# Kernel tuning notes

Hardware: AMD Instinct MI355X
Metric: run time of the kernel (lower is better)

## Reference

```python
import jax, jax.numpy as jnp
import numpy as np

# dims (Nemotron-H 8B class mamba mixer)
HID = 4096      # hidden_size
NH = 128        # mamba_num_heads
HD = 64         # mamba_head_dim
DIN = NH * HD   # intermediate_size = 8192
G = 8           # n_groups
N = 128         # ssm_state_size
K = 4           # conv_kernel
CS = 256        # chunk_size
EPS = 1e-5
GROUP_SIZE = DIN // G
CONV_DIM = DIN + 2 * G * N           # 10240
PROJ = DIN + CONV_DIM + NH           # 18560 = gate | xBC | dt


def segment_sum(x):
    """x: [..., k] -> [..., k, k]; out[i,j] = sum_{m=j+1..i} x[m], -inf above diag."""
    k = x.shape[-1]
    xe = jnp.broadcast_to(x[..., None], x.shape + (k,))
    xe = jnp.where(jnp.tril(jnp.ones((k, k), bool), -1), xe, 0.0)
    s = jnp.cumsum(xe, axis=-2)
    return jnp.where(jnp.tril(jnp.ones((k, k), bool), 0), s, -jnp.inf)


def setup_inputs() -> dict:
    key = jax.random.key(0)
    ks = jax.random.split(key, 9)
    std = 0.02
    return {
        "hidden_states": jax.random.normal(ks[0], (2, 2048, HID), jnp.float32),
        "in_proj_w": jax.random.normal(ks[1], (PROJ, HID), jnp.float32) * std,
        "conv_w": jax.random.normal(ks[2], (CONV_DIM, 1, K), jnp.float32) * 0.1,
        "conv_b": jax.random.normal(ks[3], (CONV_DIM,), jnp.float32) * 0.01,
        "dt_bias": jax.random.uniform(ks[4], (NH,), jnp.float32, -4.0, -2.0),
        "A_log": jnp.log(jax.random.uniform(ks[5], (NH,), jnp.float32, 1.0, 16.0)),
        "D": jnp.ones((NH,), jnp.float32),
        "norm_w": jnp.ones((DIN,), jnp.float32),
        "out_proj_w": jax.random.normal(ks[8], (HID, DIN), jnp.float32) * std,
    }


def reference(hidden_states, in_proj_w, conv_w, conv_b, dt_bias, A_log, D, norm_w, out_proj_w):
    b, l, _ = hidden_states.shape
    zxbcdt = hidden_states @ in_proj_w.T                       # [b,l,PROJ]
    gate = zxbcdt[..., :DIN]
    xBC = zxbcdt[..., DIN:DIN + CONV_DIM]
    dt = zxbcdt[..., DIN + CONV_DIM:]                          # [b,l,NH]

    # causal depthwise conv1d + silu
    conv = jax.lax.conv_general_dilated(
        jnp.transpose(xBC, (0, 2, 1)), conv_w, (1,), [(K - 1, 0)],
        feature_group_count=CONV_DIM, dimension_numbers=("NCH", "OIH", "NCH"))
    xBC = jax.nn.silu(jnp.transpose(conv + conv_b[None, :, None], (0, 2, 1)))

    x = xBC[..., :DIN].reshape(b, l, NH, HD)
    B = xBC[..., DIN:DIN + G * N].reshape(b, l, G, N)
    C = xBC[..., DIN + G * N:].reshape(b, l, G, N)
    B = jnp.repeat(B, NH // G, axis=2)                         # [b,l,NH,N]
    C = jnp.repeat(C, NH // G, axis=2)

    A = -jnp.exp(A_log)                                        # [NH]
    dt = jax.nn.softplus(dt + dt_bias)                         # [b,l,NH]; limit (0,inf) is a no-op

    pad = (CS - l % CS) % CS
    def padl(t):
        return jnp.pad(t, [(0, 0), (0, pad)] + [(0, 0)] * (t.ndim - 2))

    D_res = D[None, None, :, None] * padl(x)                   # [b,L,NH,HD]
    xs = x * dt[..., None]
    Adt = A[None, None, :] * dt                                # [b,l,NH]

    nc = (l + pad) // CS
    def chunk(t):
        return padl(t).reshape((b, nc, CS) + t.shape[2:])
    xs, B, C = chunk(xs), chunk(B), chunk(C)                   # [b,c,k,h,*]
    Ac = jnp.transpose(chunk(Adt), (0, 3, 1, 2))               # [b,h,c,k]
    A_cumsum = jnp.cumsum(Ac, axis=-1)

    # 1. intra-chunk (diagonal blocks)
    L = jnp.exp(segment_sum(Ac))                               # [b,h,c,k,k]
    Gm = jnp.einsum("bcihn,bcjhn->bhcij", C, B)
    Y_diag = jnp.einsum("bhcij,bcjhd->bcihd", Gm * L, xs)

    # 2. chunk states
    decay_states = jnp.exp(A_cumsum[..., -1:] - A_cumsum)      # [b,h,c,k]
    states = jnp.einsum("bckhn,bhck,bckhd->bchdn", B, decay_states, xs)

    # 3. inter-chunk recurrence
    A_tail = jnp.pad(A_cumsum[..., -1], ((0, 0), (0, 0), (1, 0)))
    decay_chunk = jnp.exp(segment_sum(A_tail))                 # [b,h,c+1,c+1]
    states = jnp.concatenate([jnp.zeros_like(states[:, :1]), states], axis=1)
    new_states = jnp.einsum("bhzc,bchdn->bzhdn", decay_chunk, states)
    states = new_states[:, :-1]                                # [b,c,h,d,n]

    # 4. state -> output
    state_decay = jnp.exp(A_cumsum)                            # [b,h,c,k]
    Y_off = jnp.einsum("bckhn,bchdn,bhck->bckhd", C, states, state_decay)

    y = (Y_diag + Y_off).reshape(b, l + pad, NH, HD) + D_res
    y = y[:, :l].reshape(b, l, DIN)

    # gated grouped RMSNorm
    y = y * jax.nn.silu(gate)
    yg = y.reshape(b, l, G, GROUP_SIZE)
    var = jnp.mean(yg * yg, axis=-1, keepdims=True)
    y = (yg * jax.lax.rsqrt(var + EPS)).reshape(b, l, DIN) * norm_w
    return y @ out_proj_w.T
```

## Files before the change

kernel.cpp:

```cpp
#include <hip/hip_runtime.h>
#include <hip/hip_bf16.h>
#include <math.h>

#define HID 4096
#define NH 128
#define HD 64
#define DIN 8192
#define G 8
#define NSTATE 128
#define CS 256
#define GROUP_SIZE 1024
#define CONV_DIM 10240
#define ZXW 18432
#define BATCH 2
#define SEQ 2048
#define NT (BATCH*SEQ)
#define NC 8
#define DTSK 16

typedef __attribute__((ext_vector_type(8))) short bf16x8;
typedef __attribute__((ext_vector_type(4))) float f32x4;
typedef __attribute__((ext_vector_type(8))) unsigned short u16x8;
typedef __attribute__((ext_vector_type(4))) unsigned short u16x4;

__device__ __forceinline__ float sigmoidf_(float x){ return 1.f/(1.f+expf(-x)); }
__device__ __forceinline__ float siluf_(float x){ return x*sigmoidf_(x); }
__device__ __forceinline__ float softplusf_(float x){ return (x>20.f)? x : log1pf(expf(x)); }
__device__ __forceinline__ float b2f(unsigned short u){ union{unsigned int i; float f;} x; x.i = ((unsigned int)u)<<16; return x.f; }
__device__ __forceinline__ unsigned short f2b(float f){ __hip_bfloat16 h = __float2bfloat16(f); return *(unsigned short*)&h; }

__device__ __forceinline__ void gload_lds16(const void* g, void* l) {
  __builtin_amdgcn_global_load_lds((const __attribute__((address_space(1))) unsigned int*)g,
                                   (__attribute__((address_space(3))) unsigned int*)l, 16, 0, 0);
}
__device__ __forceinline__ bf16x8 ld8bf(const __hip_bfloat16* p){ return *(const bf16x8*)p; }

__device__ __forceinline__ void cast8(const float* in, __hip_bfloat16* out) {
  const float4* p = (const float4*)in;
  float4 a = p[0], b = p[1];
  union { __hip_bfloat16 h[8]; int4 v; } o;
  o.h[0]=__float2bfloat16(a.x); o.h[1]=__float2bfloat16(a.y);
  o.h[2]=__float2bfloat16(a.z); o.h[3]=__float2bfloat16(a.w);
  o.h[4]=__float2bfloat16(b.x); o.h[5]=__float2bfloat16(b.y);
  o.h[6]=__float2bfloat16(b.z); o.h[7]=__float2bfloat16(b.w);
  *(int4*)out = o.v;
}

__global__ __launch_bounds__(256)
void cast2_kernel(const float* __restrict__ w_in, __hip_bfloat16* __restrict__ w_in_bf,
                  const float* __restrict__ w_out, __hip_bfloat16* __restrict__ w_out_bf) {
  const size_t n1 = (size_t)ZXW*HID/8;
  const size_t n2 = (size_t)HID*DIN/8;
  const size_t ntot = n1 + n2;
  size_t i = (size_t)blockIdx.x * 256 + threadIdx.x;
  size_t stride = (size_t)gridDim.x * 256;
  for (; i < ntot; i += stride) {
    if (i < n1)  cast8(w_in + i*8,      w_in_bf + i*8);
    else         cast8(w_out+ (i-n1)*8, w_out_bf+ (i-n1)*8);
  }
}

template<bool OUT_BF16>
__global__ __launch_bounds__(512)
void gemm_bf16_256(const __hip_bfloat16* __restrict__ A, const __hip_bfloat16* __restrict__ B,
                   void* __restrict__ Cout, int M, int N, int K) {
  const int nMt = M >> 8, nNt = N >> 8;
  const int nwg = nMt * nNt;
  const int cpx = nwg >> 3;
  const int lin = blockIdx.x;
  const int swz = (lin & 7) * cpx + (lin >> 3);
  const int mt = swz % nMt, ntile = swz / nMt;
  const int rowBase = mt << 8;
  const int colBase = ntile << 8;

  __shared__ short As[4][8192];
  __shared__ short Bs[4][8192];

  const int tid = threadIdx.x;
  const int lane = tid & 63, wid = tid >> 6;
  const int wr = wid >> 2, wc = wid & 3;
  const int l15 = lane & 15, l4 = lane >> 4;

  const int r0 = tid >> 2,        c0 = (tid & 3) ^ ((r0 >> 1) & 3);
  const int r1 = (512+tid) >> 2,  c1 = ((512+tid) & 3) ^ ((r1 >> 1) & 3);
  const __hip_bfloat16* gA0 = A + (size_t)(rowBase + r0)*K + c0*8;
  const __hip_bfloat16* gA1 = A + (size_t)(rowBase + r1)*K + c1*8;
  const __hip_bfloat16* gB0 = B + (size_t)(colBase + r0)*K + c0*8;
  const __hip_bfloat16* gB1 = B + (size_t)(colBase + r1)*K + c1*8;
  const int ld0 = wid*512, ld1 = 4096 + wid*512;

#define STAGE_A(q, kt) do { \
    gload_lds16(gA0 + (size_t)(kt)*32, (void*)&As[q][ld0]); \
    gload_lds16(gA1 + (size_t)(kt)*32, (void*)&As[q][ld1]); \
  } while(0)
#define STAGE_B(q, kt) do { \
    gload_lds16(gB0 + (size_t)(kt)*32, (void*)&Bs[q][ld0]); \
    gload_lds16(gB1 + (size_t)(kt)*32, (void*)&Bs[q][ld1]); \
  } while(0)

  int aoff[8], boff[4];
  #pragma unroll
  for (int m=0;m<8;++m){ int r = wr*128 + m*16 + l15; aoff[m] = r*32 + ((l4 ^ ((r>>1)&3))*8); }
  #pragma unroll
  for (int n=0;n<4;++n){ int r = wc*64  + n*16 + l15; boff[n] = r*32 + ((l4 ^ ((r>>1)&3))*8); }

  f32x4 acc[8][4] = {};
  const int NKT = K >> 5;

  STAGE_A(0,0); STAGE_B(0,0);
  STAGE_A(1,1); STAGE_B(1,1);
  STAGE_A(2,2); STAGE_B(2,2);
  asm volatile("s_waitcnt vmcnt(8)" ::: "memory");
  __builtin_amdgcn_s_barrier();

  for (int t = 0; t < NKT; ++t) {
    const short* ab = &As[t&3][0];
    const short* bb = &Bs[t&3][0];
    const int q3 = (t+3)&3;
    bf16x8 a[4], b[4], a2[4];
    #pragma unroll
    for (int m=0;m<4;++m) a[m] = *(const bf16x8*)&ab[aoff[m]];
    #pragma unroll
    for (int n=0;n<4;++n) b[n] = *(const bf16x8*)&bb[boff[n]];
    if (t + 3 < NKT) STAGE_A(q3, t+3);
    __builtin_amdgcn_s_barrier();
    asm volatile("s_waitcnt lgkmcnt(0)" ::: "memory");
    __builtin_amdgcn_sched_barrier(0);
    __builtin_amdgcn_s_setprio(1);
    #pragma unroll
    for (int m=0;m<4;++m)
      #pragma unroll
      for (int n=0;n<4;++n)
        acc[m][n] = __builtin_amdgcn_mfma_f32_16x16x32_bf16(a[m], b[n], acc[m][n], 0, 0, 0);
    __builtin_amdgcn_s_setprio(0);
    __builtin_amdgcn_s_barrier();
    #pragma unroll
    for (int m=0;m<4;++m) a2[m] = *(const bf16x8*)&ab[aoff[m+4]];
    if (t + 3 < NKT) STAGE_B(q3, t+3);
    const int rem = NKT - 1 - t;
    if (rem >= 3)      asm volatile("s_waitcnt vmcnt(8)" ::: "memory");
    else if (rem == 2) asm volatile("s_waitcnt vmcnt(4)" ::: "memory");
    else if (rem == 1) asm volatile("s_waitcnt vmcnt(0)" ::: "memory");
    __builtin_amdgcn_s_barrier();
    asm volatile("s_waitcnt lgkmcnt(0)" ::: "memory");
    __builtin_amdgcn_sched_barrier(0);
    __builtin_amdgcn_s_setprio(1);
    #pragma unroll
    for (int m=0;m<4;++m)
      #pragma unroll
      for (int n=0;n<4;++n)
        acc[m+4][n] = __builtin_amdgcn_mfma_f32_16x16x32_bf16(a2[m], b[n], acc[m+4][n], 0, 0, 0);
    __builtin_amdgcn_s_setprio(0);
    __builtin_amdgcn_s_barrier();
  }
#undef STAGE_A
#undef STAGE_B

  #pragma unroll
  for (int m=0;m<8;++m) {
    int row0 = rowBase + wr*128 + m*16 + l4*4;
    #pragma unroll
    for (int n=0;n<4;++n) {
      int col = colBase + wc*64 + n*16 + l15;
      #pragma unroll
      for (int j=0;j<4;++j) {
        if (OUT_BF16)
          ((__hip_bfloat16*)Cout)[(size_t)(row0+j)*N + col] = __float2bfloat16(acc[m][n][j]);
        else
          ((float*)Cout)[(size_t)(row0+j)*N + col] = acc[m][n][j];
      }
    }
  }
}

__global__ __launch_bounds__(256)
void dt_gemm_splitk(const float* __restrict__ A, const float* __restrict__ B,
                    float* __restrict__ partial, __hip_bfloat16* __restrict__ hs_bf) {
  __shared__ float As[16][132];
  __shared__ float Bs[16][132];
  const int tid = threadIdx.x;
  const int tx = tid & 15, ty = tid >> 4;
  const int rowBase = blockIdx.y * 128;
  const int k0 = blockIdx.x * (HID/DTSK);
  float acc[8][8] = {};
  for (int kt = k0; kt < k0 + HID/DTSK; kt += 16) {
    for (int e = tid; e < 128*16; e += 256) {
      int r = e >> 4, c = e & 15;
      float av = A[(size_t)(rowBase + r) * HID + kt + c];
      As[c][r] = av;
      hs_bf[(size_t)(rowBase + r) * HID + kt + c] = __float2bfloat16(av);
      Bs[c][r] = B[(size_t)r * HID + kt + c];
    }
    __syncthreads();
    #pragma unroll
    for (int kk = 0; kk < 16; ++kk) {
      float a[8], bv[8];
      #pragma unroll
      for (int i = 0; i < 8; ++i) a[i] = As[kk][ty*8+i];
      #pragma unroll
      for (int j = 0; j < 8; ++j) bv[j] = Bs[kk][tx*8+j];
      #pragma unroll
      for (int i = 0; i < 8; ++i)
        #pragma unroll
        for (int j = 0; j < 8; ++j)
          acc[i][j] += a[i]*bv[j];
    }
    __syncthreads();
  }
  float* outp = partial + (size_t)blockIdx.x * NT * NH;
  for (int i = 0; i < 8; ++i) {
    size_t ro = (size_t)(rowBase + ty*8 + i) * NH + tx*8;
    #pragma unroll
    for (int j = 0; j < 8; ++j) outp[ro + j] = acc[i][j];
  }
}

__global__ __launch_bounds__(256)
void dt_scan_kernel(const float* __restrict__ partial, const float* __restrict__ dt_bias,
                    const float* __restrict__ A_log, float* __restrict__ dt_sp,
                    float* __restrict__ Acs) {
  int bid = blockIdx.x;
  int c = bid % NC;
  int h = (bid / NC) % NH;
  int b = bid / (NC*NH);
  int k = threadIdx.x;
  int t = b*SEQ + c*CS + k;
  float raw = dt_bias[h];
  #pragma unroll
  for (int sk = 0; sk < DTSK; ++sk) raw += partial[(size_t)sk*NT*NH + (size_t)t*NH + h];
  float dtv = softplusf_(raw);
  dt_sp[(size_t)t*NH + h] = dtv;
  float adt = -expf(A_log[h]) * dtv;
  __shared__ float s[CS];
  s[k] = adt;
  __syncthreads();
  for (int off = 1; off < CS; off <<= 1) {
    float v = (k >= off) ? s[k-off] : 0.f;
    __syncthreads();
    s[k] += v;
    __syncthreads();
  }
  Acs[((size_t)(b*NH + h)*NC + c)*CS + k] = s[k];
}

__global__ __launch_bounds__(256)
void conv_fused_kernel(const __hip_bfloat16* __restrict__ zx, const float* __restrict__ w,
                       const float* __restrict__ bias,
                       const float* __restrict__ dt_sp, const float* __restrict__ Acs,
                       __hip_bfloat16* __restrict__ xsT, __hip_bfloat16* __restrict__ xwT,
                       __hip_bfloat16* __restrict__ Bbf, __hip_bfloat16* __restrict__ Cbf,
                       __hip_bfloat16* __restrict__ BT) {
  const int tt = blockIdx.x;
  const int ct = blockIdx.y;
  const int t0 = tt*64;
  const int ch0 = ct*64;
  const int tid = threadIdx.x;
  __shared__ unsigned short T[64][72];
  __shared__ float dts[64], ews[64];

  const bool isX = (ch0 < DIN);
  const bool isB = (ch0 >= DIN) && (ch0 < DIN + G*NSTATE);

  if (isX && tid < 64) {
    int h = ch0 >> 6;
    int t = t0 + tid;
    dts[tid] = dt_sp[(size_t)t*NH + h];
    int b = t0 >> 11, cc = (t0 >> 8) & 7, k0 = t0 & 255;
    const float* acs = Acs + ((size_t)(b*NH+h)*NC + cc)*CS;
    ews[tid] = __expf(acs[CS-1] - acs[k0 + tid]);
  }

  const int l0 = t0 & (SEQ-1);
  #pragma unroll
  for (int it = 0; it < 2; ++it) {
    int r = tid >> 2;
    int c8 = (tid & 3) + it*4;
    int cb = ch0 + c8*8;
    float acc[8];
    *(float4*)&acc[0] = *(const float4*)&bias[cb];
    *(float4*)&acc[4] = *(const float4*)&bias[cb+4];
    float4 wv[8];
    #pragma unroll
    for (int q=0;q<8;++q) wv[q] = *(const float4*)&w[(cb+q)*4];
    #pragma unroll
    for (int k=0;k<4;++k) {
      if (l0 + r - 3 + k >= 0) {
        u16x8 v = *(const u16x8*)&zx[(size_t)(t0+r-3+k)*ZXW + DIN + cb];
        #pragma unroll
        for (int q=0;q<8;++q) acc[q] += b2f(v[q]) * ((const float*)&wv[q])[k];
      }
    }
    u16x8 o;
    #pragma unroll
    for (int q=0;q<8;++q) o[q] = f2b(siluf_(acc[q]));
    if (isX || isB) {
      #pragma unroll
      for (int q=0;q<8;++q) T[c8*8+q][r] = o[q];
    }
    if (!isX) {
      if (isB) *(u16x8*)&Bbf[(size_t)(t0+r)*(G*NSTATE) + (cb - DIN)] = o;
      else     *(u16x8*)&Cbf[(size_t)(t0+r)*(G*NSTATE) + (cb - DIN - G*NSTATE)] = o;
    }
  }
  if (!isX && !isB) return;
  __syncthreads();
  #pragma unroll
  for (int it = 0; it < 2; ++it) {
    int ch = tid >> 2;
    int tc = (tid & 3) + it*4;
    u16x8 v = *(const u16x8*)&T[ch][tc*8];
    if (isX) {
      u16x8 a, wv2;
      #pragma unroll
      for (int q=0;q<8;++q) {
        float f = b2f(v[q]);
        float fs = f * dts[tc*8+q];
        a[q]   = f2b(fs);
        wv2[q] = f2b(fs * ews[tc*8+q]);
      }
      *(u16x8*)&xsT[(size_t)(ch0+ch)*NT + t0 + tc*8] = a;
      *(u16x8*)&xwT[(size_t)(ch0+ch)*NT + t0 + tc*8] = wv2;
    } else {
      *(u16x8*)&BT[(size_t)(ch0 - DIN + ch)*NT + t0 + tc*8] = v;
    }
  }
}

__global__ __launch_bounds__(256)
void chunk_states_fused(const __hip_bfloat16* __restrict__ xwT, const __hip_bfloat16* __restrict__ BT,
                        const float* __restrict__ Acs, __hip_bfloat16* __restrict__ states_bf) {
  int h = blockIdx.x, b = blockIdx.y;
  int g = h >> 4;
  int tid = threadIdx.x, lane = tid & 63, w = tid >> 6;
  int l15 = lane & 15, l4 = lane >> 4;
  int n0 = w*32;
  f32x4 S[4][2] = {};
  for (int c = 0; c < NC; ++c) {
    int tbase = b*SEQ + c*CS;
    const __hip_bfloat16* xp = xwT + (size_t)(h*64 + l15)*NT + tbase + l4*8;
    const __hip_bfloat16* bp = BT + (size_t)(g*128 + n0 + l15)*NT + tbase + l4*8;
    f32x4 acc[4][2] = {};
    for (int kc = 0; kc < 8; ++kc) {
      bf16x8 xf[4], bf2[2];
      #pragma unroll
      for (int tm=0;tm<4;++tm) xf[tm] = ld8bf(xp + (size_t)(tm*16)*NT + kc*32);
      #pragma unroll
      for (int tn=0;tn<2;++tn) bf2[tn] = ld8bf(bp + (size_t)(tn*16)*NT + kc*32);
      #pragma unroll
      for (int tm=0;tm<4;++tm)
        #pragma unroll
        for (int tn=0;tn<2;++tn)
          acc[tm][tn] = __builtin_amdgcn_mfma_f32_16x16x32_bf16(xf[tm], bf2[tn], acc[tm][tn], 0, 0, 0);
    }
    __hip_bfloat16* out = states_bf + ((size_t)(b*NC + c)*NH + h)*(HD*NSTATE);
    float decay = expf(Acs[((size_t)(b*NH+h)*NC + c)*CS + CS-1]);
    #pragma unroll
    for (int tm=0;tm<4;++tm)
      #pragma unroll
      for (int tn=0;tn<2;++tn)
        #pragma unroll
        for (int q=0;q<4;++q) {
          out[(size_t)(tm*16 + l4*4 + q)*NSTATE + n0 + tn*16 + l15] = __float2bfloat16(S[tm][tn][q]);
          S[tm][tn][q] = S[tm][tn][q]*decay + acc[tm][tn][q];
        }
  }
}

__global__ __launch_bounds__(256)
void y_mfma_kernel(const __hip_bfloat16* __restrict__ zx,
                   const __hip_bfloat16* __restrict__ Cn,
                   const __hip_bfloat16* __restrict__ Bn,
                   const __hip_bfloat16* __restrict__ xsT,
                   const __hip_bfloat16* __restrict__ Sbf,
                   const float* __restrict__ dt_sp,
                   const float* __restrict__ Acs,
                   const float* __restrict__ Dp,
                   __hip_bfloat16* __restrict__ ybf) {
  int h = blockIdx.x;
  int bc = blockIdx.y;
  int c = bc & 7, b = bc >> 3;
  int g = h >> 4;
  int tbase = b*SEQ + c*CS;
  int tid = threadIdx.x, lane = tid & 63, w = tid >> 6;
  int l15 = lane & 15, l4 = lane >> 4;
  int i0 = w*64;
  __shared__ float acs_s[CS];
  __shared__ unsigned short P[4][64][72];
  acs_s[tid] = Acs[((size_t)(b*NH+h)*NC + c)*CS + tid];
  __syncthreads();

  float acs_i[4], rd[4];
  float Dh = Dp[h];
  #pragma unroll
  for (int ti=0;ti<4;++ti) {
    int ig = i0 + ti*16 + l15;
    acs_i[ti] = acs_s[ig];
    rd[ti] = Dh / dt_sp[(size_t)(tbase+ig)*NH + h];
  }
  const __hip_bfloat16* Cbase = Cn + (size_t)tbase*1024 + g*128;
  const __hip_bfloat16* Bbase = Bn + (size_t)tbase*1024 + g*128;
  const __hip_bfloat16* xbase = xsT + (size_t)(h*64 + l15)*NT + tbase;

  bf16x8 cfr[4][4];
  #pragma unroll
  for (int kc = 0; kc < 4; ++kc)
    #pragma unroll
    for (int ti=0;ti<4;++ti)
      cfr[kc][ti] = ld8bf(Cbase + (size_t)(i0 + ti*16 + l15)*1024 + kc*32 + l4*8);

  f32x4 accY[4][4] = {};
  for (int jb = 0; jb <= w; ++jb) {
    int j0 = jb*64;
    f32x4 sacc[4][4] = {};
    for (int kc = 0; kc < 4; ++kc) {
      bf16x8 bfr[4];
      #pragma unroll
      for (int tj=0;tj<4;++tj) bfr[tj] = ld8bf(Bbase + (size_t)(j0 + tj*16 + l15)*1024 + kc*32 + l4*8);
      #pragma unroll
      for (int tj=0;tj<4;++tj)
        #pragma unroll
        for (int ti=0;ti<4;++ti)
          sacc[tj][ti] = __builtin_amdgcn_mfma_f32_16x16x32_bf16(bfr[tj], cfr[kc][ti], sacc[tj][ti], 0, 0, 0);
    }
    if (jb < w) {
      #pragma unroll
      for (int tj=0;tj<4;++tj)
        #pragma unroll
        for (int ti=0;ti<4;++ti) {
          float ai = acs_i[ti];
          u16x4 pk;
          #pragma unroll
          for (int q=0;q<4;++q) {
            int jg = j0 + tj*16 + l4*4 + q;
            pk[q] = f2b(sacc[tj][ti][q] * __expf(ai - acs_s[jg]));
          }
          *(u16x4*)&P[w][ti*16 + l15][tj*16 + l4*4] = pk;
        }
    } else {
      #pragma unroll
      for (int tj=0;tj<4;++tj)
        #pragma unroll
        for (int ti=0;ti<4;++ti) {
          int ig = i0 + ti*16 + l15;
          float ai = acs_i[ti];
          u16x4 pk;
          #pragma unroll
          for (int q=0;q<4;++q) {
            int jg = j0 + tj*16 + l4*4 + q;
            float v = (jg <= ig) ? sacc[tj][ti][q] * __expf(ai - acs_s[jg]) : 0.f;
            if (jg == ig) v += rd[ti];
            pk[q] = f2b(v);
          }
          *(u16x4*)&P[w][ti*16 + l15][tj*16 + l4*4] = pk;
        }
    }
    #pragma unroll
    for (int kc2 = 0; kc2 < 2; ++kc2) {
      bf16x8 xf[4], pf[4];
      #pragma unroll
      for (int tm=0;tm<4;++tm) xf[tm] = ld8bf(xbase + (size_t)(tm*16)*NT + j0 + kc2*32 + l4*8);
      #pragma unroll
      for (int ti=0;ti<4;++ti) pf[ti] = *(const bf16x8*)&P[w][ti*16 + l15][kc2*32 + l4*8];
      #pragma unroll
      for (int tm=0;tm<4;++tm)
        #pragma unroll
        for (int ti=0;ti<4;++ti)
          accY[tm][ti] = __builtin_amdgcn_mfma_f32_16x16x32_bf16(xf[tm], pf[ti], accY[tm][ti], 0, 0, 0);
    }
  }
  const __hip_bfloat16* Sb = Sbf + ((size_t)bc*NH + h)*(HD*NSTATE);
  f32x4 oacc[4][4] = {};
  #pragma unroll
  for (int kc = 0; kc < 4; ++kc) {
    bf16x8 sf[4];
    #pragma unroll
    for (int tm=0;tm<4;++tm) sf[tm] = ld8bf(Sb + (size_t)(tm*16 + l15)*NSTATE + kc*32 + l4*8);
    #pragma unroll
    for (int tm=0;tm<4;++tm)
      #pragma unroll
      for (int ti=0;ti<4;++ti)
        oacc[tm][ti] = __builtin_amdgcn_mfma_f32_16x16x32_bf16(sf[tm], cfr[kc][ti], oacc[tm][ti], 0, 0, 0);
  }
  #pragma unroll
  for (int ti=0;ti<4;++ti) {
    int ig = i0 + ti*16 + l15;
    int t = tbase + ig;
    float sd = __expf(acs_i[ti]);
    #pragma unroll
    for (int tm=0;tm<4;++tm) {
      int ch0 = h*64 + tm*16 + l4*4;
      u16x4 gv = *(const u16x4*)&zx[(size_t)t*ZXW + ch0];
      u16x4 out;
      #pragma unroll
      for (int q=0;q<4;++q) {
        float yv = accY[tm][ti][q] + sd * oacc[tm][ti][q];
        yv *= siluf_(b2f(gv[q]));
        out[q] = f2b(yv);
      }
      *(u16x4*)&ybf[(size_t)t*DIN + ch0] = out;
    }
  }
}

__global__ __launch_bounds__(256)
void groupnorm_bf16_kernel(unsigned short* __restrict__ y, const float* __restrict__ norm_w) {
  int bid = blockIdx.x;
  int g = bid % G;
  int t = bid / G;
  unsigned short* yp = y + (size_t)t*DIN + g*GROUP_SIZE;
  int tid = threadIdx.x;
  u16x4 v = *(const u16x4*)&yp[tid*4];
  float f[4]; float ss = 0.f;
  #pragma unroll
  for (int j=0;j<4;++j) { f[j] = b2f(v[j]); ss += f[j]*f[j]; }
  #pragma unroll
  for (int off = 32; off > 0; off >>= 1) ss += __shfl_xor(ss, off);
  __shared__ float wsum[4];
  int wave = tid >> 6;
  if ((tid & 63) == 0) wsum[wave] = ss;
  __syncthreads();
  float tot = wsum[0]+wsum[1]+wsum[2]+wsum[3];
  float rs = rsqrtf(tot/(float)GROUP_SIZE + 1e-5f);
  const float* nw = norm_w + g*GROUP_SIZE + tid*4;
  u16x4 o;
  #pragma unroll
  for (int j=0;j<4;++j) o[j] = f2b(f[j] * rs * nw[j]);
  *(u16x4*)&yp[tid*4] = o;
}

extern "C" void kernel_launch(void* const* d_in, const int* in_sizes, int n_in,
                              void* d_out, int out_size, void* d_ws, size_t ws_size,
                              hipStream_t stream) {
  const float* hs        = (const float*)d_in[0];
  const float* in_proj_w = (const float*)d_in[1];
  const float* conv_w    = (const float*)d_in[2];
  const float* conv_b    = (const float*)d_in[3];
  const float* dt_bias   = (const float*)d_in[4];
  const float* A_log     = (const float*)d_in[5];
  const float* Dp        = (const float*)d_in[6];
  const float* norm_w    = (const float*)d_in[7];
  const float* out_proj_w= (const float*)d_in[8];
  float* outp = (float*)d_out;

  char* ws = (char*)d_ws;
  __hip_bfloat16* zx_bf = (__hip_bfloat16*)ws;
  char* p = ws + (size_t)NT*ZXW*2;
  __hip_bfloat16* B_bf  = (__hip_bfloat16*)p; p += (size_t)NT*G*NSTATE*2;
  __hip_bfloat16* C_bf  = (__hip_bfloat16*)p; p += (size_t)NT*G*NSTATE*2;
  __hip_bfloat16* BT    = (__hip_bfloat16*)p; p += (size_t)NT*G*NSTATE*2;
  __hip_bfloat16* y_bf  = (__hip_bfloat16*)p; p += (size_t)NT*DIN*2;
  float* dtb    = (float*)p;  p += (size_t)NT*NH*4;
  float* Acs    = (float*)p;  p += (size_t)BATCH*NH*NC*CS*4;
  float* dt_part = (float*)y_bf;
  char* F = p;
  __hip_bfloat16* w_in_bf   = (__hip_bfloat16*)F;
  __hip_bfloat16* xsT       = (__hip_bfloat16*)F;
  __hip_bfloat16* xwT       = (__hip_bfloat16*)(F + 67108864);
  __hip_bfloat16* hs_bf     = (__hip_bfloat16*)(F + 150994944);
  __hip_bfloat16* states_bf = (__hip_bfloat16*)(F + 150994944);
  char* F2 = F + 150994944 + 33554432;
  __hip_bfloat16* w_out_bf  = (__hip_bfloat16*)F2;

  dt_gemm_splitk<<<dim3(DTSK, NT/128), 256, 0, stream>>>(hs, in_proj_w + (size_t)ZXW*HID, dt_part, hs_bf);
  dt_scan_kernel<<<BATCH*NH*NC, CS, 0, stream>>>(dt_part, dt_bias, A_log, dtb, Acs);

  cast2_kernel<<<4096, 256, 0, stream>>>(in_proj_w, w_in_bf, out_proj_w, w_out_bf);

  gemm_bf16_256<true><<<dim3((NT/256)*(ZXW/256)), 512, 0, stream>>>(
      hs_bf, w_in_bf, zx_bf, NT, ZXW, HID);

  conv_fused_kernel<<<dim3(NT/64, CONV_DIM/64), 256, 0, stream>>>(
      zx_bf, conv_w, conv_b, dtb, Acs, xsT, xwT, B_bf, C_bf, BT);

  chunk_states_fused<<<dim3(NH, BATCH), 256, 0, stream>>>(xwT, BT, Acs, states_bf);

  y_mfma_kernel<<<dim3(NH, BATCH*NC), 256, 0, stream>>>(zx_bf, C_bf, B_bf, xsT, states_bf, dtb, Acs, Dp, y_bf);
  groupnorm_bf16_kernel<<<NT*G, 256, 0, stream>>>((unsigned short*)y_bf, norm_w);

  gemm_bf16_256<false><<<dim3((NT/256)*(HID/256)), 512, 0, stream>>>(
      y_bf, w_out_bf, outp, NT, HID, DIN);
}
```

Measured before the change: 1.728 ms.

## Simplify GEMM main loop to one barrier per k-step with merged staging

Result: slower. 1.991 ms (+15.2%).

```diff
diff --git a/kernel.cpp b/kernel.cpp
--- a/kernel.cpp
+++ b/kernel.cpp
@@ -89,11 +89,9 @@
   const __hip_bfloat16* gB1 = B + (size_t)(colBase + r1)*K + c1*8;
   const int ld0 = wid*512, ld1 = 4096 + wid*512;
 
-#define STAGE_A(q, kt) do { \
+#define STAGE(q, kt) do { \
     gload_lds16(gA0 + (size_t)(kt)*32, (void*)&As[q][ld0]); \
     gload_lds16(gA1 + (size_t)(kt)*32, (void*)&As[q][ld1]); \
-  } while(0)
-#define STAGE_B(q, kt) do { \
     gload_lds16(gB0 + (size_t)(kt)*32, (void*)&Bs[q][ld0]); \
     gload_lds16(gB1 + (size_t)(kt)*32, (void*)&Bs[q][ld1]); \
   } while(0)
@@ -107,54 +105,32 @@
   f32x4 acc[8][4] = {};
   const int NKT = K >> 5;
 
-  STAGE_A(0,0); STAGE_B(0,0);
-  STAGE_A(1,1); STAGE_B(1,1);
-  STAGE_A(2,2); STAGE_B(2,2);
-  asm volatile("s_waitcnt vmcnt(8)" ::: "memory");
-  __builtin_amdgcn_s_barrier();
+  STAGE(0,0); STAGE(1,1); STAGE(2,2);
 
   for (int t = 0; t < NKT; ++t) {
+    const int rem = NKT - 1 - t;
+    if (rem >= 2)      asm volatile("s_waitcnt vmcnt(8)" ::: "memory");
+    else if (rem == 1) asm volatile("s_waitcnt vmcnt(4)" ::: "memory");
+    else               asm volatile("s_waitcnt vmcnt(0)" ::: "memory");
+    __builtin_amdgcn_s_barrier();
+    __builtin_amdgcn_sched_barrier(0);
+    if (t + 3 < NKT) STAGE((t+3)&3, t+3);
     const short* ab = &As[t&3][0];
     const short* bb = &Bs[t&3][0];
-    const int q3 = (t+3)&3;
-    bf16x8 a[4], b[4], a2[4];
-    #pragma unroll
-    for (int m=0;m<4;++m) a[m] = *(const bf16x8*)&ab[aoff[m]];
+    bf16x8 a[8], b[4];
     #pragma unroll
     for (int n=0;n<4;++n) b[n] = *(const bf16x8*)&bb[boff[n]];
-    if (t + 3 < NKT) STAGE_A(q3, t+3);
-    __builtin_amdgcn_s_barrier();
-    asm volatile("s_waitcnt lgkmcnt(0)" ::: "memory");
-    __builtin_amdgcn_sched_barrier(0);
+    #pragma unroll
+    for (int m=0;m<8;++m) a[m] = *(const bf16x8*)&ab[aoff[m]];
     __builtin_amdgcn_s_setprio(1);
     #pragma unroll
-    for (int m=0;m<4;++m)
+    for (int m=0;m<8;++m)
       #pragma unroll
       for (int n=0;n<4;++n)
         acc[m][n] = __builtin_amdgcn_mfma_f32_16x16x32_bf16(a[m], b[n], acc[m][n], 0, 0, 0);
     __builtin_amdgcn_s_setprio(0);
-    __builtin_amdgcn_s_barrier();
-    #pragma unroll
-    for (int m=0;m<4;++m) a2[m] = *(const bf16x8*)&ab[aoff[m+4]];
-    if (t + 3 < NKT) STAGE_B(q3, t+3);
-    const int rem = NKT - 1 - t;
-    if (rem >= 3)      asm volatile("s_waitcnt vmcnt(8)" ::: "memory");
-    else if (rem == 2) asm volatile("s_waitcnt vmcnt(4)" ::: "memory");
-    else if (rem == 1) asm volatile("s_waitcnt vmcnt(0)" ::: "memory");
-    __builtin_amdgcn_s_barrier();
-    asm volatile("s_waitcnt lgkmcnt(0)" ::: "memory");
-    __builtin_amdgcn_sched_barrier(0);
-    __builtin_amdgcn_s_setprio(1);
-    #pragma unroll
-    for (int m=0;m<4;++m)
-      #pragma unroll
-      for (int n=0;n<4;++n)
-        acc[m+4][n] = __builtin_amdgcn_mfma_f32_16x16x32_bf16(a2[m], b[n], acc[m+4][n], 0, 0, 0);
-    __builtin_amdgcn_s_setprio(0);
-    __builtin_amdgcn_s_barrier();
-  }
-#undef STAGE_A
-#undef STAGE_B
+  }
+#undef STAGE
 
   #pragma unroll
   for (int m=0;m<8;++m) {
```

## Fuse weight cast into dt GEMM and rebalance causal y kernel tiles

Applied to the files above, without the earlier changes.

Result: faster. 1.646 ms (median of 2 runs) (-4.8%).

```diff
diff --git a/kernel.cpp b/kernel.cpp
--- a/kernel.cpp
+++ b/kernel.cpp
@@ -46,20 +46,6 @@
   *(int4*)out = o.v;
 }
 
-__global__ __launch_bounds__(256)
-void cast2_kernel(const float* __restrict__ w_in, __hip_bfloat16* __restrict__ w_in_bf,
-                  const float* __restrict__ w_out, __hip_bfloat16* __restrict__ w_out_bf) {
-  const size_t n1 = (size_t)ZXW*HID/8;
-  const size_t n2 = (size_t)HID*DIN/8;
-  const size_t ntot = n1 + n2;
-  size_t i = (size_t)blockIdx.x * 256 + threadIdx.x;
-  size_t stride = (size_t)gridDim.x * 256;
-  for (; i < ntot; i += stride) {
-    if (i < n1)  cast8(w_in + i*8,      w_in_bf + i*8);
-    else         cast8(w_out+ (i-n1)*8, w_out_bf+ (i-n1)*8);
-  }
-}
-
 template<bool OUT_BF16>
 __global__ __launch_bounds__(512)
 void gemm_bf16_256(const __hip_bfloat16* __restrict__ A, const __hip_bfloat16* __restrict__ B,
@@ -175,7 +161,9 @@
 
 __global__ __launch_bounds__(256)
 void dt_gemm_splitk(const float* __restrict__ A, const float* __restrict__ B,
-                    float* __restrict__ partial, __hip_bfloat16* __restrict__ hs_bf) {
+                    float* __restrict__ partial, __hip_bfloat16* __restrict__ hs_bf,
+                    const float* __restrict__ w_in, __hip_bfloat16* __restrict__ w_in_bf,
+                    const float* __restrict__ w_out, __hip_bfloat16* __restrict__ w_out_bf) {
   __shared__ float As[16][132];
   __shared__ float Bs[16][132];
   const int tid = threadIdx.x;
@@ -212,6 +200,17 @@
     size_t ro = (size_t)(rowBase + ty*8 + i) * NH + tx*8;
     #pragma unroll
     for (int j = 0; j < 8; ++j) outp[ro + j] = acc[i][j];
+  }
+  {
+    const size_t n1 = (size_t)ZXW*HID/8;
+    const size_t n2 = (size_t)HID*DIN/8;
+    const size_t ntot = n1 + n2;
+    size_t gid = ((size_t)blockIdx.y * gridDim.x + blockIdx.x) * 256 + tid;
+    size_t gsz = (size_t)gridDim.x * gridDim.y * 256;
+    for (size_t i = gid; i < ntot; i += gsz) {
+      if (i < n1)  cast8(w_in + i*8,      w_in_bf + i*8);
+      else         cast8(w_out+ (i-n1)*8, w_out_bf+ (i-n1)*8);
+    }
   }
 }
 
@@ -383,121 +382,121 @@
   int tbase = b*SEQ + c*CS;
   int tid = threadIdx.x, lane = tid & 63, w = tid >> 6;
   int l15 = lane & 15, l4 = lane >> 4;
-  int i0 = w*64;
   __shared__ float acs_s[CS];
-  __shared__ unsigned short P[4][64][72];
+  __shared__ unsigned short P[4][32][40];
   acs_s[tid] = Acs[((size_t)(b*NH+h)*NC + c)*CS + tid];
   __syncthreads();
 
-  float acs_i[4], rd[4];
   float Dh = Dp[h];
-  #pragma unroll
-  for (int ti=0;ti<4;++ti) {
-    int ig = i0 + ti*16 + l15;
-    acs_i[ti] = acs_s[ig];
-    rd[ti] = Dh / dt_sp[(size_t)(tbase+ig)*NH + h];
-  }
   const __hip_bfloat16* Cbase = Cn + (size_t)tbase*1024 + g*128;
   const __hip_bfloat16* Bbase = Bn + (size_t)tbase*1024 + g*128;
   const __hip_bfloat16* xbase = xsT + (size_t)(h*64 + l15)*NT + tbase;
-
-  bf16x8 cfr[4][4];
-  #pragma unroll
-  for (int kc = 0; kc < 4; ++kc)
-    #pragma unroll
-    for (int ti=0;ti<4;++ti)
-      cfr[kc][ti] = ld8bf(Cbase + (size_t)(i0 + ti*16 + l15)*1024 + kc*32 + l4*8);
-
-  f32x4 accY[4][4] = {};
-  for (int jb = 0; jb <= w; ++jb) {
-    int j0 = jb*64;
-    f32x4 sacc[4][4] = {};
+  const __hip_bfloat16* Sb = Sbf + ((size_t)bc*NH + h)*(HD*NSTATE);
+
+  for (int tix = 0; tix < 2; ++tix) {
+    const int kt = tix ? (7 - w) : w;
+    const int i0 = kt * 32;
+    float acs_i[2], rd2[2];
+    #pragma unroll
+    for (int ti=0;ti<2;++ti) {
+      int ig = i0 + ti*16 + l15;
+      acs_i[ti] = acs_s[ig];
+      rd2[ti] = Dh / dt_sp[(size_t)(tbase+ig)*NH + h];
+    }
+    bf16x8 cfr[4][2];
+    #pragma unroll
+    for (int kc = 0; kc < 4; ++kc)
+      #pragma unroll
+      for (int ti=0;ti<2;++ti)
+        cfr[kc][ti] = ld8bf(Cbase + (size_t)(i0 + ti*16 + l15)*1024 + kc*32 + l4*8);
+
+    f32x4 accY[4][2] = {};
+    for (int jb = 0; jb <= kt; ++jb) {
+      int j0 = jb*32;
+      f32x4 sacc[2][2] = {};
+      for (int kc = 0; kc < 4; ++kc) {
+        bf16x8 bfr[2];
+        #pragma unroll
+        for (int tj=0;tj<2;++tj) bfr[tj] = ld8bf(Bbase + (size_t)(j0 + tj*16 + l15)*1024 + kc*32 + l4*8);
+        #pragma unroll
+        for (int tj=0;tj<2;++tj)
+          #pragma unroll
+          for (int ti=0;ti<2;++ti)
+            sacc[tj][ti] = __builtin_amdgcn_mfma_f32_16x16x32_bf16(bfr[tj], cfr[kc][ti], sacc[tj][ti], 0, 0, 0);
+      }
+      if (jb < kt) {
+        #pragma unroll
+        for (int tj=0;tj<2;++tj)
+          #pragma unroll
+          for (int ti=0;ti<2;++ti) {
+            float ai = acs_i[ti];
+            u16x4 pk;
+            #pragma unroll
+            for (int q=0;q<4;++q) {
+              int jg = j0 + tj*16 + l4*4 + q;
+              pk[q] = f2b(sacc[tj][ti][q] * __expf(ai - acs_s[jg]));
+            }
+            *(u16x4*)&P[w][ti*16 + l15][tj*16 + l4*4] = pk;
+          }
+      } else {
+        #pragma unroll
+        for (int tj=0;tj<2;++tj)
+          #pragma unroll
+          for (int ti=0;ti<2;++ti) {
+            int ig = i0 + ti*16 + l15;
+            float ai = acs_i[ti];
+            u16x4 pk;
+            #pragma unroll
+            for (int q=0;q<4;++q) {
+              int jg = j0 + tj*16 + l4*4 + q;
+              float v = (jg <= ig) ? sacc[tj][ti][q] * __expf(ai - acs_s[jg]) : 0.f;
+              if (jg == ig) v += rd2[ti];
+              pk[q] = f2b(v);
+            }
+            *(u16x4*)&P[w][ti*16 + l15][tj*16 + l4*4] = pk;
+          }
+      }
+      bf16x8 xf[4], pf[2];
+      #pragma unroll
+      for (int tm=0;tm<4;++tm) xf[tm] = ld8bf(xbase + (size_t)(tm*16)*NT + j0 + l4*8);
+      #pragma unroll
+      for (int ti=0;ti<2;++ti) pf[ti] = *(const bf16x8*)&P[w][ti*16 + l15][l4*8];
+      #pragma unroll
+      for (int tm=0;tm<4;++tm)
+        #pragma unroll
+        for (int ti=0;ti<2;++ti)
+          accY[tm][ti] = __builtin_amdgcn_mfma_f32_16x16x32_bf16(xf[tm], pf[ti], accY[tm][ti], 0, 0, 0);
+    }
+    f32x4 oacc[4][2] = {};
+    #pragma unroll
     for (int kc = 0; kc < 4; ++kc) {
-      bf16x8 bfr[4];
-      #pragma unroll
-      for (int tj=0;tj<4;++tj) bfr[tj] = ld8bf(Bbase + (size_t)(j0 + tj*16 + l15)*1024 + kc*32 + l4*8);
-      #pragma unroll
-      for (int tj=0;tj<4;++tj)
-        #pragma unroll
-        for (int ti=0;ti<4;++ti)
-          sacc[tj][ti] = __builtin_amdgcn_mfma_f32_16x16x32_bf16(bfr[tj], cfr[kc][ti], sacc[tj][ti], 0, 0, 0);
-    }
-    if (jb < w) {
-      #pragma unroll
-      for (int tj=0;tj<4;++tj)
-        #pragma unroll
-        for (int ti=0;ti<4;++ti) {
-          float ai = acs_i[ti];
-          u16x4 pk;
-          #pragma unroll
-          for (int q=0;q<4;++q) {
-            int jg = j0 + tj*16 + l4*4 + q;
-            pk[q] = f2b(sacc[tj][ti][q] * __expf(ai - acs_s[jg]));
-          }
-          *(u16x4*)&P[w][ti*16 + l15][tj*16 + l4*4] = pk;
+      bf16x8 sf[4];
+      #pragma unroll
+      for (int tm=0;tm<4;++tm) sf[tm] = ld8bf(Sb + (size_t)(tm*16 + l15)*NSTATE + kc*32 + l4*8);
+      #pragma unroll
+      for (int tm=0;tm<4;++tm)
+        #pragma unroll
+        for (int ti=0;ti<2;++ti)
+          oacc[tm][ti] = __builtin_amdgcn_mfma_f32_16x16x32_bf16(sf[tm], cfr[kc][ti], oacc[tm][ti], 0, 0, 0);
+    }
+    #pragma unroll
+    for (int ti=0;ti<2;++ti) {
+      int ig = i0 + ti*16 + l15;
+      int t = tbase + ig;
+      float sd = __expf(acs_i[ti]);
+      #pragma unroll
+      for (int tm=0;tm<4;++tm) {
+        int ch0 = h*64 + tm*16 + l4*4;
+        u16x4 gv = *(const u16x4*)&zx[(size_t)t*ZXW + ch0];
+        u16x4 out;
+        #pragma unroll
+        for (int q=0;q<4;++q) {
+          float yv = accY[tm][ti][q] + sd * oacc[tm][ti][q];
+          yv *= siluf_(b2f(gv[q]));
+          out[q] = f2b(yv);
         }
-    } else {
-      #pragma unroll
-      for (int tj=0;tj<4;++tj)
-        #pragma unroll
-        for (int ti=0;ti<4;++ti) {
-          int ig = i0 + ti*16 + l15;
-          float ai = acs_i[ti];
-          u16x4 pk;
-          #pragma unroll
-          for (int q=0;q<4;++q) {
-            int jg = j0 + tj*16 + l4*4 + q;
-            float v = (jg <= ig) ? sacc[tj][ti][q] * __expf(ai - acs_s[jg]) : 0.f;
-            if (jg == ig) v += rd[ti];
-            pk[q] = f2b(v);
-          }
-          *(u16x4*)&P[w][ti*16 + l15][tj*16 + l4*4] = pk;
-        }
-    }
-    #pragma unroll
-    for (int kc2 = 0; kc2 < 2; ++kc2) {
-      bf16x8 xf[4], pf[4];
-      #pragma unroll
-      for (int tm=0;tm<4;++tm) xf[tm] = ld8bf(xbase + (size_t)(tm*16)*NT + j0 + kc2*32 + l4*8);
-      #pragma unroll
-      for (int ti=0;ti<4;++ti) pf[ti] = *(const bf16x8*)&P[w][ti*16 + l15][kc2*32 + l4*8];
-      #pragma unroll
-      for (int tm=0;tm<4;++tm)
-        #pragma unroll
-        for (int ti=0;ti<4;++ti)
-          accY[tm][ti] = __builtin_amdgcn_mfma_f32_16x16x32_bf16(xf[tm], pf[ti], accY[tm][ti], 0, 0, 0);
-    }
-  }
-  const __hip_bfloat16* Sb = Sbf + ((size_t)bc*NH + h)*(HD*NSTATE);
-  f32x4 oacc[4][4] = {};
-  #pragma unroll
-  for (int kc = 0; kc < 4; ++kc) {
-    bf16x8 sf[4];
-    #pragma unroll
-    for (int tm=0;tm<4;++tm) sf[tm] = ld8bf(Sb + (size_t)(tm*16 + l15)*NSTATE + kc*32 + l4*8);
-    #pragma unroll
-    for (int tm=0;tm<4;++tm)
-      #pragma unroll
-      for (int ti=0;ti<4;++ti)
-        oacc[tm][ti] = __builtin_amdgcn_mfma_f32_16x16x32_bf16(sf[tm], cfr[kc][ti], oacc[tm][ti], 0, 0, 0);
-  }
-  #pragma unroll
-  for (int ti=0;ti<4;++ti) {
-    int ig = i0 + ti*16 + l15;
-    int t = tbase + ig;
-    float sd = __expf(acs_i[ti]);
-    #pragma unroll
-    for (int tm=0;tm<4;++tm) {
-      int ch0 = h*64 + tm*16 + l4*4;
-      u16x4 gv = *(const u16x4*)&zx[(size_t)t*ZXW + ch0];
-      u16x4 out;
-      #pragma unroll
-      for (int q=0;q<4;++q) {
-        float yv = accY[tm][ti][q] + sd * oacc[tm][ti][q];
-        yv *= siluf_(b2f(gv[q]));
-        out[q] = f2b(yv);
+        *(u16x4*)&ybf[(size_t)t*DIN + ch0] = out;
       }
-      *(u16x4*)&ybf[(size_t)t*DIN + ch0] = out;
     }
   }
 }
@@ -561,10 +560,10 @@
   char* F2 = F + 150994944 + 33554432;
   __hip_bfloat16* w_out_bf  = (__hip_bfloat16*)F2;
 
-  dt_gemm_splitk<<<dim3(DTSK, NT/128), 256, 0, stream>>>(hs, in_proj_w + (size_t)ZXW*HID, dt_part, hs_bf);
+  dt_gemm_splitk<<<dim3(DTSK, NT/128), 256, 0, stream>>>(
+      hs, in_proj_w + (size_t)ZXW*HID, dt_part, hs_bf,
+      in_proj_w, w_in_bf, out_proj_w, w_out_bf);
   dt_scan_kernel<<<BATCH*NH*NC, CS, 0, stream>>>(dt_part, dt_bias, A_log, dtb, Acs);
-
-  cast2_kernel<<<4096, 256, 0, stream>>>(in_proj_w, w_in_bf, out_proj_w, w_out_bf);
 
   gemm_bf16_256<true><<<dim3((NT/256)*(ZXW/256)), 512, 0, stream>>>(
       hs_bf, w_in_bf, zx_bf, NT, ZXW, HID);
```
